# Performance work log

Measured on AMD Instinct MI355X. Metric: run time of the kernel, lower is better.

The kernel has to match this reference:

```python
import jax, jax.numpy as jnp
import numpy as np

B, T, I, H = 64, 512, 1024, 1024


def setup_inputs() -> dict:
    key = jax.random.key(0)
    ks = jax.random.split(key, 8)
    s = 0.02
    return {
        "x": jax.random.normal(ks[0], (B, T, I), dtype=jnp.float32),
        "h_0": jax.random.normal(ks[1], (B, H), dtype=jnp.float32),
        "W_ih": jax.random.normal(ks[2], (H, I), dtype=jnp.float32) * s,
        "b_ih": jax.random.normal(ks[3], (H,), dtype=jnp.float32) * s,
        "W_hh1": jax.random.normal(ks[4], (H, H), dtype=jnp.float32) * s,
        "b_hh1": jax.random.normal(ks[5], (H,), dtype=jnp.float32) * s,
        "W_hh2": jax.random.normal(ks[6], (H, H), dtype=jnp.float32) * s,
        "b_hh2": jax.random.normal(ks[7], (H,), dtype=jnp.float32) * s,
    }


def reference(x, h_0, W_ih, b_ih, W_hh1, b_hh1, W_hh2, b_hh2):
    # Shared input projection is time-independent: hoist out of the scan.
    # xp: [B, T, H]
    xp = jnp.einsum("bti,hi->bth", x, W_ih) + b_ih

    def step(h, xp_t):
        # xp_t: [B, H], h: [B, H]
        v1 = jnp.tanh(xp_t + h @ W_hh1.T + b_hh1)
        v2 = jnp.tanh(xp_t + h @ W_hh2.T + b_hh2)
        h_new = (1.0 - h) * v1 + h * v2
        return h_new, h_new

    h_T, ys = jax.lax.scan(step, h_0, jnp.swapaxes(xp, 0, 1))  # ys: [T, B, H]
    out = jnp.swapaxes(ys, 0, 1)  # [B, T, H]
    # nn.Dropout is identity in eval mode; reference is deterministic.
    return out, h_T
```

## Files before the change

kernel.cpp:

```cpp
#include <hip/hip_runtime.h>

using u32 = unsigned int;
using u64 = unsigned long long;
using bf16x8 = __attribute__((ext_vector_type(8))) short;
using f32x4  = __attribute__((ext_vector_type(4))) float;

#define BB_ 64
#define TT_ 512
#define II_ 1024
#define HH_ 1024
#define NSCAN_BLOCKS 128
#define DOM 32

__device__ __forceinline__ unsigned short bf16rne(float f) {
  u32 u = __float_as_uint(f);
  return (unsigned short)((u + 0x7FFFu + ((u >> 16) & 1u)) >> 16);
}
__device__ __forceinline__ u32 pk2(float a, float b) {
  u32 ua = __float_as_uint(a), ub = __float_as_uint(b);
  u32 lo = (ua + 0x7FFFu + ((ua >> 16) & 1u)) >> 16;
  u32 hi = (ub + 0x7FFFu + ((ub >> 16) & 1u)) & 0xFFFF0000u;
  return lo | hi;
}
__device__ __forceinline__ void gll16(const void* g, void* s) {
  __builtin_amdgcn_global_load_lds(
      (const __attribute__((address_space(1))) u32*)g,
      (__attribute__((address_space(3))) u32*)s, 16, 0, 0);
}

__device__ __forceinline__ void cvt4(const float* __restrict__ s, unsigned short* __restrict__ d, long long g) {
  float4 v = ((const float4*)s)[g];
  ushort4 o;
  o.x = bf16rne(v.x); o.y = bf16rne(v.y); o.z = bf16rne(v.z); o.w = bf16rne(v.w);
  ((ushort4*)d)[g] = o;
}

__global__ void k_convert(const float* __restrict__ x, const float* __restrict__ h0,
                          const float* __restrict__ Wih, const float* __restrict__ Wh1,
                          const float* __restrict__ Wh2,
                          unsigned short* __restrict__ xb, unsigned short* __restrict__ Wihb,
                          unsigned short* __restrict__ Wcatb, unsigned short* __restrict__ hbuf,
                          int* __restrict__ cnt, int do_x) {
  const long long NWI = (long long)HH_ * II_ / 4;
  const long long NH0 = (long long)BB_ * HH_ / 4;
  const long long NC  = 128;
  const long long NX  = do_x ? ((long long)BB_ * TT_ * II_ / 4) : 0;
  const long long total = 3 * NWI + NH0 + NC + NX;
  for (long long g = (long long)blockIdx.x * blockDim.x + threadIdx.x; g < total;
       g += (long long)gridDim.x * blockDim.x) {
    if (g < NWI) {
      cvt4(Wih, Wihb, g);
    } else if (g < 2 * NWI) {
      cvt4(Wh1, Wcatb, g - NWI);
    } else if (g < 3 * NWI) {
      cvt4(Wh2, Wcatb + (long long)HH_ * II_, g - 2 * NWI);
    } else if (g < 3 * NWI + NH0) {
      cvt4(h0, hbuf, g - 3 * NWI);
    } else if (g < 3 * NWI + NH0 + NC) {
      ((int4*)cnt)[g - 3 * NWI - NH0] = make_int4(0, 0, 0, 0);
    } else {
      cvt4(x, xb, g - (3 * NWI + NH0 + NC));
    }
  }
}

template <bool XB>
__global__ __launch_bounds__(256) void k_gemm(const unsigned short* __restrict__ xbg,
                                              const float* __restrict__ xf,
                                              const unsigned short* __restrict__ Wb,
                                              const float* __restrict__ bias,
                                              float* __restrict__ C) {
  __shared__ __align__(16) unsigned short ldsA[128 * 64];
  __shared__ __align__(16) unsigned short ldsB[128 * 64];
  const int tid = threadIdx.x;
  const int w = tid >> 6, l = tid & 63;
  const int lr = l & 15, lk = l >> 4;
  const int n0 = (blockIdx.x & 7) * 128;
  const int m0 = (blockIdx.x >> 3) * 128;
  const int mbase = (w >> 1) * 64, nbase = (w & 1) * 64;

  f32x4 acc[4][4] = {};

  for (int kb = 0; kb < 16; ++kb) {
    const int k0 = kb * 64;
#pragma unroll
    for (int r = 0; r < 4; ++r) {
      int tb = r * 4096 + w * 1024 + l * 16;
      int row = tb >> 7;
      int p = (tb >> 4) & 7;
      int c = p ^ (row & 7);
      gll16(Wb + (u64)(n0 + row) * II_ + k0 + c * 8,
            (char*)ldsB + r * 4096 + w * 1024);
    }
    if constexpr (XB) {
#pragma unroll
      for (int r = 0; r < 4; ++r) {
        int tb = r * 4096 + w * 1024 + l * 16;
        int row = tb >> 7;
        int p = (tb >> 4) & 7;
        int c = p ^ (row & 7);
        gll16(xbg + (u64)(m0 + row) * II_ + k0 + c * 8,
              (char*)ldsA + r * 4096 + w * 1024);
      }
    } else {
      const int r = tid >> 1, ch = tid & 1;
      const float* gs = xf + (u64)(m0 + r) * II_ + k0 + ch * 32;
      float4 v[8];
#pragma unroll
      for (int q = 0; q < 8; ++q) v[q] = ((const float4*)gs)[q];
#pragma unroll
      for (int q = 0; q < 4; ++q) {
        int c = ch * 4 + q;
        int p = c ^ (r & 7);
        uint4 pk;
        pk.x = pk2(v[2 * q].x, v[2 * q].y);
        pk.y = pk2(v[2 * q].z, v[2 * q].w);
        pk.z = pk2(v[2 * q + 1].x, v[2 * q + 1].y);
        pk.w = pk2(v[2 * q + 1].z, v[2 * q + 1].w);
        *(uint4*)((char*)ldsA + r * 128 + p * 16) = pk;
      }
    }
    __syncthreads();

    bf16x8 a[4][2], b[4][2];
#pragma unroll
    for (int mt = 0; mt < 4; ++mt) {
      int row = mbase + mt * 16 + lr;
#pragma unroll
      for (int kk = 0; kk < 2; ++kk) {
        int c = kk * 4 + lk, p = c ^ (row & 7);
        a[mt][kk] = *(const bf16x8*)((const char*)ldsA + row * 128 + p * 16);
      }
    }
#pragma unroll
    for (int nt = 0; nt < 4; ++nt) {
      int row = nbase + nt * 16 + lr;
#pragma unroll
      for (int kk = 0; kk < 2; ++kk) {
        int c = kk * 4 + lk, p = c ^ (row & 7);
        b[nt][kk] = *(const bf16x8*)((const char*)ldsB + row * 128 + p * 16);
      }
    }
#pragma unroll
    for (int kk = 0; kk < 2; ++kk)
#pragma unroll
      for (int mt = 0; mt < 4; ++mt)
#pragma unroll
        for (int nt = 0; nt < 4; ++nt)
          acc[mt][nt] = __builtin_amdgcn_mfma_f32_16x16x32_bf16(a[mt][kk], b[nt][kk], acc[mt][nt], 0, 0, 0);
    __syncthreads();
  }

  float bn[4];
#pragma unroll
  for (int nt = 0; nt < 4; ++nt) bn[nt] = bias[n0 + nbase + nt * 16 + lr];
#pragma unroll
  for (int mt = 0; mt < 4; ++mt) {
#pragma unroll
    for (int i = 0; i < 4; ++i) {
      int m = m0 + mbase + mt * 16 + lk * 4 + i;
      float* cr = C + (u64)m * HH_ + n0 + nbase + lr;
#pragma unroll
      for (int nt = 0; nt < 4; ++nt) cr[nt * 16] = acc[mt][nt][i] + bn[nt];
    }
  }
}

__global__ __launch_bounds__(256) void k_scan(float* __restrict__ out, const float* __restrict__ h0,
                                              const float* __restrict__ b1, const float* __restrict__ b2,
                                              const unsigned short* __restrict__ Wcat,
                                              unsigned short* __restrict__ hbuf, u32* __restrict__ flag) {
  __shared__ __align__(16) float part[4 * 4 * 4 * 64];
  __shared__ __align__(8) unsigned short hstage[16 * 32];
  const int tid = threadIdx.x, w = tid >> 6, l = tid & 63;
  const int lr = l & 15, lk = l >> 4;
  const int og = blockIdx.x & 31, bg = blockIdx.x >> 5;
  const int jb = og * 32, bb = bg * 16;
  const int koff = w * 256;

  bf16x8 wt[4][8];
#pragma unroll
  for (int nt = 0; nt < 4; ++nt) {
    int nrow = (nt < 2) ? (jb + nt * 16 + lr) : (HH_ + jb + (nt - 2) * 16 + lr);
    const unsigned short* wr = Wcat + (u64)nrow * HH_ + koff + lk * 8;
#pragma unroll
    for (int kk = 0; kk < 8; ++kk) wt[nt][kk] = *(const bf16x8*)(wr + kk * 32);
  }

  const int jj = w & 1, i0 = (w >> 1) * 2;
  const int jloc = jj * 16 + lr;
  const int jcol = jb + jloc;
  const float bvA = b1[jcol], bvB = b2[jcol];
  float hold[2];
#pragma unroll
  for (int q = 0; q < 2; ++q)
    hold[q] = h0[(u64)(bb + lk * 4 + i0 + q) * HH_ + jcol];

  u32* dflag = flag + bg * DOM;
  const u64 b4 = ((u64)(bb + lr) * HH_ + koff + lk * 8) >> 2;

  for (int t = 0; t < TT_; ++t) {
    float xpv[2];
#pragma unroll
    for (int q = 0; q < 2; ++q)
      xpv[q] = out[((u64)(bb + lk * 4 + i0 + q) * TT_ + t) * HH_ + jcol];

    if (t > 0) {
      if (w == 0) {
        const u32 need = (u32)t;
        while (true) {
          u32 v = (l < DOM)
                      ? __hip_atomic_load(dflag + l, __ATOMIC_RELAXED, __HIP_MEMORY_SCOPE_AGENT)
                      : 0xFFFFFFFFu;
          if (__all((int)(v >= need))) break;
        }
      }
      __syncthreads();
    }

    const u64* hB = (const u64*)hbuf + (u64)(t & 1) * (BB_ * HH_ / 4);
    u64 qv[16];
#pragma unroll
    for (int kk = 0; kk < 8; ++kk) {
      qv[2 * kk]     = __hip_atomic_load(hB + b4 + kk * 8,     __ATOMIC_RELAXED, __HIP_MEMORY_SCOPE_AGENT);
      qv[2 * kk + 1] = __hip_atomic_load(hB + b4 + kk * 8 + 1, __ATOMIC_RELAXED, __HIP_MEMORY_SCOPE_AGENT);
    }

    f32x4 acc[4] = {};
#pragma unroll
    for (int kk = 0; kk < 8; ++kk) {
      union { u64 q[2]; bf16x8 v; } au;
      au.q[0] = qv[2 * kk]; au.q[1] = qv[2 * kk + 1];
#pragma unroll
      for (int nt = 0; nt < 4; ++nt)
        acc[nt] = __builtin_amdgcn_mfma_f32_16x16x32_bf16(au.v, wt[nt][kk], acc[nt], 0, 0, 0);
    }

#pragma unroll
    for (int nt = 0; nt < 4; ++nt)
#pragma unroll
      for (int i = 0; i < 4; ++i)
        part[((w * 4 + nt) * 4 + i) * 64 + l] = acc[nt][i];
    __syncthreads();

    float hn2[2];
#pragma unroll
    for (int q = 0; q < 2; ++q) {
      const int i = i0 + q;
      float v1 = 0.f, v2 = 0.f;
#pragma unroll
      for (int ww = 0; ww < 4; ++ww) {
        v1 += part[((ww * 4 + jj) * 4 + i) * 64 + l];
        v2 += part[((ww * 4 + jj + 2) * 4 + i) * 64 + l];
      }
      float s1 = v1 + xpv[q] + bvA;
      float s2 = v2 + xpv[q] + bvB;
      float t1 = tanhf(s1), t2 = tanhf(s2);
      float h = hold[q];
      float hn = t1 + h * (t2 - t1);
      hold[q] = hn;
      hn2[q] = hn;
      out[((u64)(bb + lk * 4 + i) * TT_ + t) * HH_ + jcol] = hn;
      hstage[(lk * 4 + i) * 32 + jloc] = bf16rne(hn);
    }
    if (t == TT_ - 1) {
#pragma unroll
      for (int q = 0; q < 2; ++q)
        out[(u64)BB_ * TT_ * HH_ + (u64)(bb + lk * 4 + i0 + q) * HH_ + jcol] = hn2[q];
    }
    __syncthreads();

    if (t < TT_ - 1) {
      if (tid < 128) {
        const int m = tid >> 3, c4 = tid & 7;
        u64 v = *(const u64*)&hstage[m * 32 + c4 * 4];
        u64* dst = (u64*)hbuf + (u64)((t + 1) & 1) * (BB_ * HH_ / 4) +
                   (((u64)(bb + m) * HH_ + jb + c4 * 4) >> 2);
        __hip_atomic_store(dst, v, __ATOMIC_RELAXED, __HIP_MEMORY_SCOPE_AGENT);
      }
      asm volatile("s_waitcnt vmcnt(0)" ::: "memory");
      __syncthreads();
      if (tid == 0)
        __hip_atomic_store(dflag + og, (u32)(t + 1), __ATOMIC_RELAXED, __HIP_MEMORY_SCOPE_AGENT);
    }
  }
}

extern "C" void kernel_launch(void* const* d_in, const int* in_sizes, int n_in,
                              void* d_out, int out_size, void* d_ws, size_t ws_size,
                              hipStream_t stream) {
  const float* x    = (const float*)d_in[0];
  const float* h0   = (const float*)d_in[1];
  const float* Wih  = (const float*)d_in[2];
  const float* bih  = (const float*)d_in[3];
  const float* Whh1 = (const float*)d_in[4];
  const float* bhh1 = (const float*)d_in[5];
  const float* Whh2 = (const float*)d_in[6];
  const float* bhh2 = (const float*)d_in[7];
  float* out = (float*)d_out;

  char* ws = (char*)d_ws;
  unsigned short* Wihb  = (unsigned short*)(ws + 0);
  unsigned short* Wcatb = (unsigned short*)(ws + 2097152);
  unsigned short* hbuf  = (unsigned short*)(ws + 6291456);
  int*            cnt   = (int*)(ws + 6553600);
  unsigned short* xb    = (unsigned short*)(ws + 6555648);
  const bool fastx = ws_size >= 73664512ULL;

  hipLaunchKernelGGL(k_convert, dim3(2048), dim3(256), 0, stream,
                     x, h0, Wih, Whh1, Whh2, xb, Wihb, Wcatb, hbuf, cnt, (int)fastx);
  if (fastx)
    hipLaunchKernelGGL((k_gemm<true>), dim3(2048), dim3(256), 0, stream,
                       xb, (const float*)nullptr, Wihb, bih, out);
  else
    hipLaunchKernelGGL((k_gemm<false>), dim3(2048), dim3(256), 0, stream,
                       (const unsigned short*)nullptr, x, Wihb, bih, out);
  hipLaunchKernelGGL(k_scan, dim3(NSCAN_BLOCKS), dim3(256), 0, stream,
                     out, h0, bhh1, bhh2, Wcatb, hbuf, (u32*)cnt);
}
```

Measured before the change: 2.336 ms.

## Split scan over 256 blocks with 8 batch rows each and fast tanh

The persistent scan kernel now runs 256 blocks, each handling 8 batch rows by 32 hidden columns instead of 16 by 32. The upper half of each MFMA A operand is zeroed, so half the MFMA work is padding, but each block's recurrent slice is smaller. Other changes: weights are kept in AGPRs through inline asm MFMA, the waiting loop runs in every wave with s_sleep instead of a barrier, tanhf is replaced by an exp2-based approximation, the new hidden state is packed and stored straight from registers through lane shuffles, and the flag store uses release ordering. The aim is to cut per-timestep latency on the serial critical path. The risks are the approximate tanh and more polling traffic from 256 blocks.

```diff
diff --git a/kernel.cpp b/kernel.cpp
--- a/kernel.cpp
+++ b/kernel.cpp
@@ -9,8 +9,7 @@
 #define TT_ 512
 #define II_ 1024
 #define HH_ 1024
-#define NSCAN_BLOCKS 128
-#define DOM 32
+#define NSCAN_BLOCKS 256
 
 __device__ __forceinline__ unsigned short bf16rne(float f) {
   u32 u = __float_as_uint(f);
@@ -26,6 +25,10 @@
   __builtin_amdgcn_global_load_lds(
       (const __attribute__((address_space(1))) u32*)g,
       (__attribute__((address_space(3))) u32*)s, 16, 0, 0);
+}
+__device__ __forceinline__ float tanhfast(float x) {
+  float e = __builtin_amdgcn_exp2f(x * 2.885390081777927f);
+  return 1.0f - 2.0f / (e + 1.0f);
 }
 
 __device__ __forceinline__ void cvt4(const float* __restrict__ s, unsigned short* __restrict__ d, long long g) {
@@ -169,13 +172,13 @@
 __global__ __launch_bounds__(256) void k_scan(float* __restrict__ out, const float* __restrict__ h0,
                                               const float* __restrict__ b1, const float* __restrict__ b2,
                                               const unsigned short* __restrict__ Wcat,
-                                              unsigned short* __restrict__ hbuf, u32* __restrict__ flag) {
-  __shared__ __align__(16) float part[4 * 4 * 4 * 64];
-  __shared__ __align__(8) unsigned short hstage[16 * 32];
+                                              unsigned short* __restrict__ hbuf, u32* __restrict__ flags) {
+  __shared__ float part[4 * 4 * 8 * 16];
   const int tid = threadIdx.x, w = tid >> 6, l = tid & 63;
   const int lr = l & 15, lk = l >> 4;
-  const int og = blockIdx.x & 31, bg = blockIdx.x >> 5;
-  const int jb = og * 32, bb = bg * 16;
+  const int g = blockIdx.x & 7, r = blockIdx.x >> 3;
+  const int bb = g * 8;
+  const int jb = r * 32;
   const int koff = w * 256;
 
   bf16x8 wt[4][8];
@@ -187,102 +190,85 @@
     for (int kk = 0; kk < 8; ++kk) wt[nt][kk] = *(const bf16x8*)(wr + kk * 32);
   }
 
-  const int jj = w & 1, i0 = (w >> 1) * 2;
-  const int jloc = jj * 16 + lr;
-  const int jcol = jb + jloc;
-  const float bvA = b1[jcol], bvB = b2[jcol];
-  float hold[2];
-#pragma unroll
-  for (int q = 0; q < 2; ++q)
-    hold[q] = h0[(u64)(bb + lk * 4 + i0 + q) * HH_ + jcol];
-
-  u32* dflag = flag + bg * DOM;
-  const u64 b4 = ((u64)(bb + lr) * HH_ + koff + lk * 8) >> 2;
+  const int m = tid >> 5, jc = tid & 31;
+  const int grow = bb + m, gcol = jb + jc;
+  const float bvA = b1[gcol], bvB = b2[gcol];
+  float hold = h0[(u64)grow * HH_ + gcol];
+  float* outp = out + (u64)grow * TT_ * HH_ + gcol;
+
+  u32* gflag = flags + g * 32;
+  const u64 ldw = ((u64)(bb + (lr & 7)) * HH_ + koff + lk * 8) >> 2;
+  const u64 hstw = ((u64)grow * HH_ + gcol) >> 1;
 
   for (int t = 0; t < TT_; ++t) {
-    float xpv[2];
-#pragma unroll
-    for (int q = 0; q < 2; ++q)
-      xpv[q] = out[((u64)(bb + lk * 4 + i0 + q) * TT_ + t) * HH_ + jcol];
+    float xpv = outp[(u64)t * HH_];
 
     if (t > 0) {
-      if (w == 0) {
-        const u32 need = (u32)t;
-        while (true) {
-          u32 v = (l < DOM)
-                      ? __hip_atomic_load(dflag + l, __ATOMIC_RELAXED, __HIP_MEMORY_SCOPE_AGENT)
-                      : 0xFFFFFFFFu;
-          if (__all((int)(v >= need))) break;
-        }
-      }
-      __syncthreads();
-    }
-
-    const u64* hB = (const u64*)hbuf + (u64)(t & 1) * (BB_ * HH_ / 4);
-    u64 qv[16];
-#pragma unroll
-    for (int kk = 0; kk < 8; ++kk) {
-      qv[2 * kk]     = __hip_atomic_load(hB + b4 + kk * 8,     __ATOMIC_RELAXED, __HIP_MEMORY_SCOPE_AGENT);
-      qv[2 * kk + 1] = __hip_atomic_load(hB + b4 + kk * 8 + 1, __ATOMIC_RELAXED, __HIP_MEMORY_SCOPE_AGENT);
-    }
-
+      const u32 need = (u32)t;
+      while (true) {
+        u32 v = (l < 32)
+                    ? __hip_atomic_load(gflag + l, __ATOMIC_RELAXED, __HIP_MEMORY_SCOPE_AGENT)
+                    : 0xFFFFFFFFu;
+        if (__all((int)(v >= need))) break;
+        __builtin_amdgcn_s_sleep(1);
+      }
+    }
+
+    const u64* hB = (const u64*)hbuf + (u64)(t & 1) * (BB_ * HH_ / 4) + ldw;
     f32x4 acc[4] = {};
 #pragma unroll
     for (int kk = 0; kk < 8; ++kk) {
       union { u64 q[2]; bf16x8 v; } au;
-      au.q[0] = qv[2 * kk]; au.q[1] = qv[2 * kk + 1];
+      au.q[0] = __hip_atomic_load(hB + kk * 8,     __ATOMIC_RELAXED, __HIP_MEMORY_SCOPE_AGENT);
+      au.q[1] = __hip_atomic_load(hB + kk * 8 + 1, __ATOMIC_RELAXED, __HIP_MEMORY_SCOPE_AGENT);
+      if (lr >= 8) { au.q[0] = 0; au.q[1] = 0; }
 #pragma unroll
       for (int nt = 0; nt < 4; ++nt)
-        acc[nt] = __builtin_amdgcn_mfma_f32_16x16x32_bf16(au.v, wt[nt][kk], acc[nt], 0, 0, 0);
-    }
-
-#pragma unroll
-    for (int nt = 0; nt < 4; ++nt)
-#pragma unroll
-      for (int i = 0; i < 4; ++i)
-        part[((w * 4 + nt) * 4 + i) * 64 + l] = acc[nt][i];
+        asm("v_mfma_f32_16x16x32_bf16 %0, %1, %2, %0"
+            : "+v"(acc[nt]) : "v"(au.v), "a"(wt[nt][kk]));
+    }
+    asm volatile("s_nop 7\n\ts_nop 7"
+                 :: "v"(acc[0][0]), "v"(acc[1][0]), "v"(acc[2][0]), "v"(acc[3][0]));
+
+    if (lk < 2) {
+#pragma unroll
+      for (int nt = 0; nt < 4; ++nt)
+#pragma unroll
+        for (int i = 0; i < 4; ++i)
+          part[((w * 4 + nt) * 8 + lk * 4 + i) * 16 + lr] = acc[nt][i];
+    }
     __syncthreads();
 
-    float hn2[2];
-#pragma unroll
-    for (int q = 0; q < 2; ++q) {
-      const int i = i0 + q;
-      float v1 = 0.f, v2 = 0.f;
-#pragma unroll
-      for (int ww = 0; ww < 4; ++ww) {
-        v1 += part[((ww * 4 + jj) * 4 + i) * 64 + l];
-        v2 += part[((ww * 4 + jj + 2) * 4 + i) * 64 + l];
-      }
-      float s1 = v1 + xpv[q] + bvA;
-      float s2 = v2 + xpv[q] + bvB;
-      float t1 = tanhf(s1), t2 = tanhf(s2);
-      float h = hold[q];
-      float hn = t1 + h * (t2 - t1);
-      hold[q] = hn;
-      hn2[q] = hn;
-      out[((u64)(bb + lk * 4 + i) * TT_ + t) * HH_ + jcol] = hn;
-      hstage[(lk * 4 + i) * 32 + jloc] = bf16rne(hn);
-    }
-    if (t == TT_ - 1) {
-#pragma unroll
-      for (int q = 0; q < 2; ++q)
-        out[(u64)BB_ * TT_ * HH_ + (u64)(bb + lk * 4 + i0 + q) * HH_ + jcol] = hn2[q];
-    }
-    __syncthreads();
+    const int nti = jc >> 4, c = jc & 15;
+    float v1 = 0.f, v2 = 0.f;
+#pragma unroll
+    for (int ww = 0; ww < 4; ++ww) {
+      v1 += part[((ww * 4 + nti) * 8 + m) * 16 + c];
+      v2 += part[((ww * 4 + 2 + nti) * 8 + m) * 16 + c];
+    }
+
+    float t1 = tanhfast(v1 + xpv + bvA);
+    float t2 = tanhfast(v2 + xpv + bvB);
+    float hn = t1 + hold * (t2 - t1);
+    hold = hn;
 
     if (t < TT_ - 1) {
-      if (tid < 128) {
-        const int m = tid >> 3, c4 = tid & 7;
-        u64 v = *(const u64*)&hstage[m * 32 + c4 * 4];
-        u64* dst = (u64*)hbuf + (u64)((t + 1) & 1) * (BB_ * HH_ / 4) +
-                   (((u64)(bb + m) * HH_ + jb + c4 * 4) >> 2);
-        __hip_atomic_store(dst, v, __ATOMIC_RELAXED, __HIP_MEMORY_SCOPE_AGENT);
+      u32 hb16 = (u32)bf16rne(hn);
+      u32 nb16 = (u32)__shfl_xor((int)hb16, 1);
+      if ((jc & 1) == 0) {
+        u32 wd = hb16 | (nb16 << 16);
+        __hip_atomic_store((u32*)hbuf + (u64)((t + 1) & 1) * (BB_ * HH_ / 2) + hstw, wd,
+                           __ATOMIC_RELAXED, __HIP_MEMORY_SCOPE_AGENT);
       }
       asm volatile("s_waitcnt vmcnt(0)" ::: "memory");
       __syncthreads();
       if (tid == 0)
-        __hip_atomic_store(dflag + og, (u32)(t + 1), __ATOMIC_RELAXED, __HIP_MEMORY_SCOPE_AGENT);
-    }
+        __hip_atomic_store(gflag + r, (u32)(t + 1), __ATOMIC_RELEASE, __HIP_MEMORY_SCOPE_AGENT);
+    } else {
+      out[(u64)BB_ * TT_ * HH_ + (u64)grow * HH_ + gcol] = hn;
+      __syncthreads();
+    }
+    outp[(u64)t * HH_] = hn;
   }
 }
 
```

After: 3.491 ms. 49.5% more time.
